# Optimization experiments

Hardware: AMD Instinct MI355X
Metric: run time of the kernel (lower is better)

## Reference

```python
import jax, jax.numpy as jnp
import numpy as np

DIM = 768
N_HEADS = 12
HEAD_DIM = DIM // N_HEADS
B, T = 2, 2048


def setup_inputs() -> dict:
    key = jax.random.key(0)
    ks = jax.random.split(key, 11)
    s = 0.02
    return {
        "q_in": jax.random.normal(ks[0], (B, T, DIM), jnp.float32),
        "k_in": jax.random.normal(ks[1], (B, T, DIM), jnp.float32),
        "v_in": jax.random.normal(ks[2], (B, T, DIM), jnp.float32),
        "Wq": jax.random.normal(ks[3], (DIM, DIM), jnp.float32) * s,
        "bq": jnp.zeros((DIM,), jnp.float32),
        "Wk": jax.random.normal(ks[4], (DIM, DIM), jnp.float32) * s,
        "bk": jnp.zeros((DIM,), jnp.float32),
        "Wv": jax.random.normal(ks[5], (DIM, DIM), jnp.float32) * s,
        "bv": jnp.zeros((DIM,), jnp.float32),
        "Wo": jax.random.normal(ks[6], (DIM, DIM), jnp.float32) * s,
        "bo": jnp.zeros((DIM,), jnp.float32),
    }


def reference(q_in, k_in, v_in, Wq, bq, Wk, bk, Wv, bv, Wo, bo):
    b, t, c = q_in.shape
    scale = HEAD_DIM ** -0.5
    # linear projections (torch Linear: x @ W.T + b)
    q = q_in @ Wq.T + bq
    k = k_in @ Wk.T + bk
    v = v_in @ Wv.T + bv
    # [b, t, h, d] -> [b, h, t, d]
    q = q.reshape(b, t, N_HEADS, HEAD_DIM).transpose(0, 2, 1, 3)
    k = k.reshape(b, t, N_HEADS, HEAD_DIM).transpose(0, 2, 1, 3)
    v = v.reshape(b, t, N_HEADS, HEAD_DIM).transpose(0, 2, 1, 3)
    scores = jnp.einsum("bhqd,bhkd->bhqk", q, k) * scale  # full TxT scores
    probs = jax.nn.softmax(scores, axis=-1)
    attn = jnp.einsum("bhqk,bhkd->bhqd", probs, v)
    attn = attn.transpose(0, 2, 1, 3).reshape(b, t, c)
    return attn @ Wo.T + bo
```

## Files before the change

### kernel.cpp

```cpp
#include <hip/hip_runtime.h>


typedef unsigned short u16;
typedef __attribute__((ext_vector_type(8))) short short8;
typedef __attribute__((ext_vector_type(4))) float float4v;

#define DIMC 768
#define NTOK 4096
#define NHD  12
#define HDD  64
#define SEQT 2048

__device__ __forceinline__ u16 f2bf(float f) {
  union { float f; unsigned u; } v; v.f = f;
  unsigned r = v.u + 0x7fffu + ((v.u >> 16) & 1u);
  return (u16)(r >> 16);
}
__device__ __forceinline__ float bf2f(u16 u) {
  union { unsigned u; float f; } v; v.u = ((unsigned)u) << 16;
  return v.f;
}

__global__ __launch_bounds__(256) void cvt3_kernel(
    const float* __restrict__ a, const float* __restrict__ b, const float* __restrict__ c,
    u16* __restrict__ oa, u16* __restrict__ ob, u16* __restrict__ oc) {
  int z = blockIdx.y;
  const float* s = (z == 0) ? a : (z == 1) ? b : c;
  u16* d = (z == 0) ? oa : (z == 1) ? ob : oc;
  size_t i = ((size_t)blockIdx.x * 256 + threadIdx.x) * 4;
  float4 v = *(const float4*)(s + i);
  *(ushort4*)(d + i) = make_ushort4(f2bf(v.x), f2bf(v.y), f2bf(v.z), f2bf(v.w));
}

__global__ __launch_bounds__(256) void cvt4_kernel(
    const float* __restrict__ a, const float* __restrict__ b,
    const float* __restrict__ c, const float* __restrict__ e,
    u16* __restrict__ oa, u16* __restrict__ ob, u16* __restrict__ oc, u16* __restrict__ oe) {
  int z = blockIdx.y;
  const float* s = (z == 0) ? a : (z == 1) ? b : (z == 2) ? c : e;
  u16* d = (z == 0) ? oa : (z == 1) ? ob : (z == 2) ? oc : oe;
  size_t i = ((size_t)blockIdx.x * 256 + threadIdx.x) * 4;
  float4 v = *(const float4*)(s + i);
  *(ushort4*)(d + i) = make_ushort4(f2bf(v.x), f2bf(v.y), f2bf(v.z), f2bf(v.w));
}

__device__ __forceinline__ void gemm_mainloop2(
    const u16* __restrict__ X, const u16* __restrict__ W,
    int m0, int n0, u16* Als, u16* Bls, float4v acc[4][2]) {
  int tid = threadIdx.x;
  int sr = tid >> 3, sc = (tid & 7) * 8;
  int w = tid >> 6, lane = tid & 63, quad = lane >> 4, r15 = lane & 15;
  int wm = (w >> 1) * 64, wn = (w & 1) * 32;
  const u16* xp0 = X + (size_t)(m0 + sr) * DIMC + sc;
  const u16* xp1 = xp0 + 32 * DIMC;
  const u16* xp2 = xp0 + 64 * DIMC;
  const u16* xp3 = xp0 + 96 * DIMC;
  const u16* wp0 = W + (size_t)(n0 + sr) * DIMC + sc;
  const u16* wp1 = wp0 + 32 * DIMC;
  uint4 pa0 = *(const uint4*)xp0, pa1 = *(const uint4*)xp1;
  uint4 pa2 = *(const uint4*)xp2, pa3 = *(const uint4*)xp3;
  uint4 pb0 = *(const uint4*)wp0, pb1 = *(const uint4*)wp1;
  for (int k0 = 0; k0 < DIMC; k0 += 64) {
    __syncthreads();
    *(uint4*)(Als + sr * 72 + sc) = pa0;
    *(uint4*)(Als + (sr + 32) * 72 + sc) = pa1;
    *(uint4*)(Als + (sr + 64) * 72 + sc) = pa2;
    *(uint4*)(Als + (sr + 96) * 72 + sc) = pa3;
    *(uint4*)(Bls + sr * 72 + sc) = pb0;
    *(uint4*)(Bls + (sr + 32) * 72 + sc) = pb1;
    __syncthreads();
    int kn = k0 + 64;
    if (kn < DIMC) {
      pa0 = *(const uint4*)(xp0 + kn); pa1 = *(const uint4*)(xp1 + kn);
      pa2 = *(const uint4*)(xp2 + kn); pa3 = *(const uint4*)(xp3 + kn);
      pb0 = *(const uint4*)(wp0 + kn); pb1 = *(const uint4*)(wp1 + kn);
    }
    #pragma unroll
    for (int sk = 0; sk < 2; sk++) {
      short8 af[4], bf[2];
      #pragma unroll
      for (int mf = 0; mf < 4; mf++)
        af[mf] = *(const short8*)(Als + (wm + mf * 16 + r15) * 72 + sk * 32 + quad * 8);
      #pragma unroll
      for (int nf = 0; nf < 2; nf++)
        bf[nf] = *(const short8*)(Bls + (wn + nf * 16 + r15) * 72 + sk * 32 + quad * 8);
      #pragma unroll
      for (int mf = 0; mf < 4; mf++)
        #pragma unroll
        for (int nf = 0; nf < 2; nf++)
          acc[mf][nf] = __builtin_amdgcn_mfma_f32_16x16x32_bf16(af[mf], bf[nf], acc[mf][nf], 0, 0, 0);
    }
  }
}

__global__ __launch_bounds__(256, 4) void gemm_qkv(
    const u16* __restrict__ xq, const u16* __restrict__ xk, const u16* __restrict__ xv,
    const u16* __restrict__ wq, const u16* __restrict__ wk, const u16* __restrict__ wv,
    const float* __restrict__ bq, const float* __restrict__ bk, const float* __restrict__ bv,
    u16* __restrict__ Qh, u16* __restrict__ Kh, u16* __restrict__ Vt) {
  __shared__ __align__(16) u16 Als[128 * 72];
  __shared__ __align__(16) u16 Bls[64 * 72];
  int z = blockIdx.z;
  const u16* X = (z == 0) ? xq : (z == 1) ? xk : xv;
  const u16* W = (z == 0) ? wq : (z == 1) ? wk : wv;
  const float* bias = (z == 0) ? bq : (z == 1) ? bk : bv;
  int m0 = blockIdx.x * 128, n0 = blockIdx.y * 64;
  float4v acc[4][2];
  #pragma unroll
  for (int i = 0; i < 4; i++)
    #pragma unroll
    for (int j = 0; j < 2; j++)
      #pragma unroll
      for (int r = 0; r < 4; r++) acc[i][j][r] = 0.f;
  gemm_mainloop2(X, W, m0, n0, Als, Bls, acc);
  int tid = threadIdx.x, w = tid >> 6, lane = tid & 63, quad = lane >> 4, r15 = lane & 15;
  int wm = (w >> 1) * 64, wn = (w & 1) * 32;
  #pragma unroll
  for (int mf = 0; mf < 4; mf++)
    #pragma unroll
    for (int nf = 0; nf < 2; nf++)
      #pragma unroll
      for (int rg = 0; rg < 4; rg++) {
        int m = m0 + wm + mf * 16 + quad * 4 + rg;
        int n = n0 + wn + nf * 16 + r15;
        float val = acc[mf][nf][rg] + bias[n];
        int b = m >> 11, t = m & 2047, h = n >> 6, d = n & 63;
        u16 o = f2bf(val);
        size_t bh = (size_t)(b * NHD + h);
        if (z == 2) Vt[(bh * HDD + d) * SEQT + t] = o;
        else if (z == 0) Qh[(bh * SEQT + t) * HDD + d] = o;
        else Kh[(bh * SEQT + t) * HDD + d] = o;
      }
}

__global__ __launch_bounds__(256, 3) void attn_kernel(
    const u16* __restrict__ Qh, const u16* __restrict__ Kh, const u16* __restrict__ Vt,
    u16* __restrict__ Opart, float* __restrict__ Lpart) {
  constexpr float CEXP = 0.125f * 1.44269504088896f;
  __shared__ __align__(16) u16 Kls[64 * 72];
  __shared__ __align__(16) u16 Vls[64 * 72];
  __shared__ __align__(16) u16 Pls[4 * 32 * 72];
  int bh = blockIdx.y, kv = blockIdx.z, qt0 = blockIdx.x * 128;
  int tid = threadIdx.x, w = tid >> 6, lane = tid & 63, quad = lane >> 4, r15 = lane & 15;
  int qw = qt0 + w * 32;

  short8 qa[2][2];
  #pragma unroll
  for (int qs = 0; qs < 2; qs++) {
    const u16* qp = Qh + ((size_t)bh * SEQT + qw + qs * 16 + r15) * HDD + quad * 8;
    qa[qs][0] = *(const short8*)qp;
    qa[qs][1] = *(const short8*)(qp + 32);
  }
  short8 ones;
  #pragma unroll
  for (int i = 0; i < 8; i++) ones[i] = (short)0x3F80;

  float4v oacc[2][4], lacc[2];
  #pragma unroll
  for (int qs = 0; qs < 2; qs++) {
    #pragma unroll
    for (int r = 0; r < 4; r++) lacc[qs][r] = 0.f;
    #pragma unroll
    for (int dt = 0; dt < 4; dt++)
      #pragma unroll
      for (int r = 0; r < 4; r++) oacc[qs][dt][r] = 0.f;
  }

  const u16* Kbase = Kh + (size_t)bh * SEQT * HDD;
  const u16* Vbase = Vt + (size_t)bh * HDD * SEQT;
  u16* Pw = Pls + w * (32 * 72);
  int sr = tid >> 3, sc = (tid & 7) * 8;
  int kt0 = kv * 1024;

  uint4 pk0 = *(const uint4*)(Kbase + (size_t)(kt0 + sr) * HDD + sc);
  uint4 pk1 = *(const uint4*)(Kbase + (size_t)(kt0 + sr + 32) * HDD + sc);
  uint4 pv0 = *(const uint4*)(Vbase + (size_t)sr * SEQT + kt0 + sc);
  uint4 pv1 = *(const uint4*)(Vbase + (size_t)(sr + 32) * SEQT + kt0 + sc);

  for (int it = 0; it < 16; it++) {
    __syncthreads();
    *(uint4*)(Kls + sr * 72 + sc) = pk0;
    *(uint4*)(Kls + (sr + 32) * 72 + sc) = pk1;
    *(uint4*)(Vls + sr * 72 + sc) = pv0;
    *(uint4*)(Vls + (sr + 32) * 72 + sc) = pv1;
    __syncthreads();
    int ktn = kt0 + ((it + 1) & 15) * 64;
    pk0 = *(const uint4*)(Kbase + (size_t)(ktn + sr) * HDD + sc);
    pk1 = *(const uint4*)(Kbase + (size_t)(ktn + sr + 32) * HDD + sc);
    pv0 = *(const uint4*)(Vbase + (size_t)sr * SEQT + ktn + sc);
    pv1 = *(const uint4*)(Vbase + (size_t)(sr + 32) * SEQT + ktn + sc);

    float4v st[4][2];
    #pragma unroll
    for (int nk = 0; nk < 4; nk++) {
      short8 k0 = *(const short8*)(Kls + (nk * 16 + r15) * 72 + quad * 8);
      short8 k1 = *(const short8*)(Kls + (nk * 16 + r15) * 72 + 32 + quad * 8);
      #pragma unroll
      for (int qs = 0; qs < 2; qs++) {
        float4v z;
        #pragma unroll
        for (int r = 0; r < 4; r++) z[r] = 0.f;
        z = __builtin_amdgcn_mfma_f32_16x16x32_bf16(k0, qa[qs][0], z, 0, 0, 0);
        z = __builtin_amdgcn_mfma_f32_16x16x32_bf16(k1, qa[qs][1], z, 0, 0, 0);
        st[nk][qs] = z;
      }
    }
    #pragma unroll
    for (int qs = 0; qs < 2; qs++)
      #pragma unroll
      for (int nk = 0; nk < 4; nk++) {
        float p0 = exp2f(st[nk][qs][0] * CEXP);
        float p1 = exp2f(st[nk][qs][1] * CEXP);
        float p2 = exp2f(st[nk][qs][2] * CEXP);
        float p3 = exp2f(st[nk][qs][3] * CEXP);
        unsigned lo = __builtin_amdgcn_perm(__float_as_uint(p1), __float_as_uint(p0), 0x07060302u);
        unsigned hi = __builtin_amdgcn_perm(__float_as_uint(p3), __float_as_uint(p2), 0x07060302u);
        *(uint2*)(Pw + (qs * 16 + r15) * 72 + nk * 16 + quad * 4) = make_uint2(lo, hi);
      }
    short8 pa[2][2];
    #pragma unroll
    for (int qs = 0; qs < 2; qs++) {
      pa[qs][0] = *(const short8*)(Pw + (qs * 16 + r15) * 72 + quad * 8);
      pa[qs][1] = *(const short8*)(Pw + (qs * 16 + r15) * 72 + 32 + quad * 8);
      lacc[qs] = __builtin_amdgcn_mfma_f32_16x16x32_bf16(pa[qs][0], ones, lacc[qs], 0, 0, 0);
      lacc[qs] = __builtin_amdgcn_mfma_f32_16x16x32_bf16(pa[qs][1], ones, lacc[qs], 0, 0, 0);
    }
    #pragma unroll
    for (int dt = 0; dt < 4; dt++) {
      short8 v0 = *(const short8*)(Vls + (dt * 16 + r15) * 72 + quad * 8);
      short8 v1 = *(const short8*)(Vls + (dt * 16 + r15) * 72 + 32 + quad * 8);
      #pragma unroll
      for (int qs = 0; qs < 2; qs++) {
        oacc[qs][dt] = __builtin_amdgcn_mfma_f32_16x16x32_bf16(pa[qs][0], v0, oacc[qs][dt], 0, 0, 0);
        oacc[qs][dt] = __builtin_amdgcn_mfma_f32_16x16x32_bf16(pa[qs][1], v1, oacc[qs][dt], 0, 0, 0);
      }
    }
  }
  size_t obase = ((size_t)kv * 2 * NHD + bh) * SEQT;
  #pragma unroll
  for (int qs = 0; qs < 2; qs++)
    #pragma unroll
    for (int rg = 0; rg < 4; rg++) {
      int q = qw + qs * 16 + quad * 4 + rg;
      u16* orow = Opart + (obase + q) * HDD;
      #pragma unroll
      for (int dt = 0; dt < 4; dt++) orow[dt * 16 + r15] = f2bf(oacc[qs][dt][rg]);
      if (r15 == 0) Lpart[obase + q] = lacc[qs][rg];
    }
}

__global__ __launch_bounds__(256) void merge_kernel(
    const u16* __restrict__ Opart, const float* __restrict__ Lpart, u16* __restrict__ X2) {
  int tid = threadIdx.x;
  int row = blockIdx.x * 32 + (tid >> 3);
  int dcol = (tid & 7) * 8;
  int bh = row >> 11, t = row & 2047;
  size_t off1 = (size_t)row * HDD + dcol;
  size_t off2 = off1 + (size_t)2 * NHD * SEQT * HDD;
  ushort4 a0 = *(const ushort4*)(Opart + off1);
  ushort4 a1 = *(const ushort4*)(Opart + off1 + 4);
  ushort4 b0 = *(const ushort4*)(Opart + off2);
  ushort4 b1 = *(const ushort4*)(Opart + off2 + 4);
  float inv = 1.0f / (Lpart[row] + Lpart[row + 2 * NHD * SEQT]);
  int b = bh / NHD, h = bh % NHD;
  u16 o[8];
  o[0] = f2bf((bf2f(a0.x) + bf2f(b0.x)) * inv);
  o[1] = f2bf((bf2f(a0.y) + bf2f(b0.y)) * inv);
  o[2] = f2bf((bf2f(a0.z) + bf2f(b0.z)) * inv);
  o[3] = f2bf((bf2f(a0.w) + bf2f(b0.w)) * inv);
  o[4] = f2bf((bf2f(a1.x) + bf2f(b1.x)) * inv);
  o[5] = f2bf((bf2f(a1.y) + bf2f(b1.y)) * inv);
  o[6] = f2bf((bf2f(a1.z) + bf2f(b1.z)) * inv);
  o[7] = f2bf((bf2f(a1.w) + bf2f(b1.w)) * inv);
  *(uint4*)(X2 + ((size_t)b * SEQT + t) * DIMC + h * HDD + dcol) = *(uint4*)o;
}

__global__ __launch_bounds__(256, 4) void gemm_out(
    const u16* __restrict__ X2, const u16* __restrict__ wo,
    const float* __restrict__ bo, float* __restrict__ out) {
  __shared__ __align__(16) u16 Als[128 * 72];
  __shared__ __align__(16) u16 Bls[64 * 72];
  int m0 = blockIdx.x * 128, n0 = blockIdx.y * 64;
  float4v acc[4][2];
  #pragma unroll
  for (int i = 0; i < 4; i++)
    #pragma unroll
    for (int j = 0; j < 2; j++)
      #pragma unroll
      for (int r = 0; r < 4; r++) acc[i][j][r] = 0.f;
  gemm_mainloop2(X2, wo, m0, n0, Als, Bls, acc);
  int tid = threadIdx.x, w = tid >> 6, lane = tid & 63, quad = lane >> 4, r15 = lane & 15;
  int wm = (w >> 1) * 64, wn = (w & 1) * 32;
  #pragma unroll
  for (int mf = 0; mf < 4; mf++)
    #pragma unroll
    for (int nf = 0; nf < 2; nf++)
      #pragma unroll
      for (int rg = 0; rg < 4; rg++) {
        int m = m0 + wm + mf * 16 + quad * 4 + rg;
        int n = n0 + wn + nf * 16 + r15;
        out[(size_t)m * DIMC + n] = acc[mf][nf][rg] + bo[n];
      }
}

extern "C" void kernel_launch(void* const* d_in, const int* in_sizes, int n_in,
                              void* d_out, int out_size, void* d_ws, size_t ws_size,
                              hipStream_t stream) {
  const float* q_in = (const float*)d_in[0];
  const float* k_in = (const float*)d_in[1];
  const float* v_in = (const float*)d_in[2];
  const float* Wq = (const float*)d_in[3];
  const float* bq = (const float*)d_in[4];
  const float* Wk = (const float*)d_in[5];
  const float* bk = (const float*)d_in[6];
  const float* Wv = (const float*)d_in[7];
  const float* bv = (const float*)d_in[8];
  const float* Wo = (const float*)d_in[9];
  const float* bo = (const float*)d_in[10];

  const size_t NX = (size_t)NTOK * DIMC;
  const size_t NW = (size_t)DIMC * DIMC;
  u16* ws = (u16*)d_ws;
  u16* qb = ws;
  u16* kb = qb + NX;
  u16* vb = kb + NX;
  u16* wqb = vb + NX;
  u16* wkb = wqb + NW;
  u16* wvb = wkb + NW;
  u16* wob = wvb + NW;
  u16* Qh = wob + NW;
  u16* Kh = Qh + NX;
  u16* Vt = Kh + NX;
  u16* X2 = Vt + NX;
  u16* Opart = qb;
  float* Lpart = (float*)(ws + 2 * NX);

  cvt3_kernel<<<dim3(NX / 1024, 3), 256, 0, stream>>>(q_in, k_in, v_in, qb, kb, vb);
  cvt4_kernel<<<dim3(NW / 1024, 4), 256, 0, stream>>>(Wq, Wk, Wv, Wo, wqb, wkb, wvb, wob);
  gemm_qkv<<<dim3(NTOK / 128, DIMC / 64, 3), 256, 0, stream>>>(
      qb, kb, vb, wqb, wkb, wvb, bq, bk, bv, Qh, Kh, Vt);
  attn_kernel<<<dim3(SEQT / 128, 2 * NHD, 2), 256, 0, stream>>>(Qh, Kh, Vt, Opart, Lpart);
  merge_kernel<<<dim3(2 * NHD * SEQT / 32), 256, 0, stream>>>(Opart, Lpart, X2);
  gemm_out<<<dim3(NTOK / 128, DIMC / 64), 256, 0, stream>>>(X2, wob, bo, (float*)d_out);
}
```

Before: 199.9 us.

## Split attention KV into three chunks, fold softmax scale into Q, merge convert kernels

Splits the key range of the attention kernel into three chunks (704/704/640 keys) instead of two, raising the grid from 768 to 1152 blocks for better CU fill, and extends the merge kernel to sum three partials. The softmax scale and log2e factor are folded into the Q projection epilogue, removing a multiply per score. The two conversion kernels are fused into one launch with bounds checks, and the Q-tile launch-bounds occupancy hint is dropped. Costs include more partial-output traffic in the merge and a different rounding point for the scaled Q in bf16.

```diff
diff --git a/kernel.cpp b/kernel.cpp
--- a/kernel.cpp
+++ b/kernel.cpp
@@ -10,6 +10,7 @@
 #define NHD  12
 #define HDD  64
 #define SEQT 2048
+#define CEXPQ 0.1803368757f
 
 __device__ __forceinline__ u16 f2bf(float f) {
   union { float f; unsigned u; } v; v.f = f;
@@ -21,25 +22,25 @@
   return v.f;
 }
 
-__global__ __launch_bounds__(256) void cvt3_kernel(
-    const float* __restrict__ a, const float* __restrict__ b, const float* __restrict__ c,
-    u16* __restrict__ oa, u16* __restrict__ ob, u16* __restrict__ oc) {
+__global__ __launch_bounds__(256) void cvt_all(
+    const float* __restrict__ i0, const float* __restrict__ i1, const float* __restrict__ i2,
+    const float* __restrict__ w0, const float* __restrict__ w1,
+    const float* __restrict__ w2, const float* __restrict__ w3,
+    u16* __restrict__ o0, u16* __restrict__ o1, u16* __restrict__ o2,
+    u16* __restrict__ p0, u16* __restrict__ p1, u16* __restrict__ p2, u16* __restrict__ p3) {
   int z = blockIdx.y;
-  const float* s = (z == 0) ? a : (z == 1) ? b : c;
-  u16* d = (z == 0) ? oa : (z == 1) ? ob : oc;
+  const float* s; u16* d; size_t lim;
+  switch (z) {
+    case 0: s = i0; d = o0; lim = (size_t)NTOK * DIMC; break;
+    case 1: s = i1; d = o1; lim = (size_t)NTOK * DIMC; break;
+    case 2: s = i2; d = o2; lim = (size_t)NTOK * DIMC; break;
+    case 3: s = w0; d = p0; lim = (size_t)DIMC * DIMC; break;
+    case 4: s = w1; d = p1; lim = (size_t)DIMC * DIMC; break;
+    case 5: s = w2; d = p2; lim = (size_t)DIMC * DIMC; break;
+    default: s = w3; d = p3; lim = (size_t)DIMC * DIMC; break;
+  }
   size_t i = ((size_t)blockIdx.x * 256 + threadIdx.x) * 4;
-  float4 v = *(const float4*)(s + i);
-  *(ushort4*)(d + i) = make_ushort4(f2bf(v.x), f2bf(v.y), f2bf(v.z), f2bf(v.w));
-}
-
-__global__ __launch_bounds__(256) void cvt4_kernel(
-    const float* __restrict__ a, const float* __restrict__ b,
-    const float* __restrict__ c, const float* __restrict__ e,
-    u16* __restrict__ oa, u16* __restrict__ ob, u16* __restrict__ oc, u16* __restrict__ oe) {
-  int z = blockIdx.y;
-  const float* s = (z == 0) ? a : (z == 1) ? b : (z == 2) ? c : e;
-  u16* d = (z == 0) ? oa : (z == 1) ? ob : (z == 2) ? oc : oe;
-  size_t i = ((size_t)blockIdx.x * 256 + threadIdx.x) * 4;
+  if (i >= lim) return;
   float4 v = *(const float4*)(s + i);
   *(ushort4*)(d + i) = make_ushort4(f2bf(v.x), f2bf(v.y), f2bf(v.z), f2bf(v.w));
 }
@@ -124,6 +125,7 @@
         int m = m0 + wm + mf * 16 + quad * 4 + rg;
         int n = n0 + wn + nf * 16 + r15;
         float val = acc[mf][nf][rg] + bias[n];
+        if (z == 0) val *= CEXPQ;
         int b = m >> 11, t = m & 2047, h = n >> 6, d = n & 63;
         u16 o = f2bf(val);
         size_t bh = (size_t)(b * NHD + h);
@@ -133,16 +135,17 @@
       }
 }
 
-__global__ __launch_bounds__(256, 3) void attn_kernel(
+__global__ __launch_bounds__(256) void attn_kernel(
     const u16* __restrict__ Qh, const u16* __restrict__ Kh, const u16* __restrict__ Vt,
     u16* __restrict__ Opart, float* __restrict__ Lpart) {
-  constexpr float CEXP = 0.125f * 1.44269504088896f;
   __shared__ __align__(16) u16 Kls[64 * 72];
   __shared__ __align__(16) u16 Vls[64 * 72];
   __shared__ __align__(16) u16 Pls[4 * 32 * 72];
   int bh = blockIdx.y, kv = blockIdx.z, qt0 = blockIdx.x * 128;
   int tid = threadIdx.x, w = tid >> 6, lane = tid & 63, quad = lane >> 4, r15 = lane & 15;
   int qw = qt0 + w * 32;
+  int kt0 = kv * 704;
+  int nit = (kv == 2) ? 10 : 11;
 
   short8 qa[2][2];
   #pragma unroll
@@ -166,29 +169,28 @@
       for (int r = 0; r < 4; r++) oacc[qs][dt][r] = 0.f;
   }
 
-  const u16* Kbase = Kh + (size_t)bh * SEQT * HDD;
-  const u16* Vbase = Vt + (size_t)bh * HDD * SEQT;
   u16* Pw = Pls + w * (32 * 72);
   int sr = tid >> 3, sc = (tid & 7) * 8;
-  int kt0 = kv * 1024;
-
-  uint4 pk0 = *(const uint4*)(Kbase + (size_t)(kt0 + sr) * HDD + sc);
-  uint4 pk1 = *(const uint4*)(Kbase + (size_t)(kt0 + sr + 32) * HDD + sc);
-  uint4 pv0 = *(const uint4*)(Vbase + (size_t)sr * SEQT + kt0 + sc);
-  uint4 pv1 = *(const uint4*)(Vbase + (size_t)(sr + 32) * SEQT + kt0 + sc);
-
-  for (int it = 0; it < 16; it++) {
+  const u16* pK0 = Kh + (size_t)bh * SEQT * HDD + (size_t)(kt0 + sr) * HDD + sc;
+  const u16* pK1 = pK0 + 32 * HDD;
+  const u16* pV0 = Vt + (size_t)bh * HDD * SEQT + (size_t)sr * SEQT + kt0 + sc;
+  const u16* pV1 = pV0 + 32 * SEQT;
+
+  uint4 pk0 = *(const uint4*)pK0, pk1 = *(const uint4*)pK1;
+  uint4 pv0 = *(const uint4*)pV0, pv1 = *(const uint4*)pV1;
+
+  for (int it = 0; it < nit; it++) {
     __syncthreads();
     *(uint4*)(Kls + sr * 72 + sc) = pk0;
     *(uint4*)(Kls + (sr + 32) * 72 + sc) = pk1;
     *(uint4*)(Vls + sr * 72 + sc) = pv0;
     *(uint4*)(Vls + (sr + 32) * 72 + sc) = pv1;
     __syncthreads();
-    int ktn = kt0 + ((it + 1) & 15) * 64;
-    pk0 = *(const uint4*)(Kbase + (size_t)(ktn + sr) * HDD + sc);
-    pk1 = *(const uint4*)(Kbase + (size_t)(ktn + sr + 32) * HDD + sc);
-    pv0 = *(const uint4*)(Vbase + (size_t)sr * SEQT + ktn + sc);
-    pv1 = *(const uint4*)(Vbase + (size_t)(sr + 32) * SEQT + ktn + sc);
+    if (it + 1 < nit) {
+      pK0 += 64 * HDD; pK1 += 64 * HDD; pV0 += 64; pV1 += 64;
+      pk0 = *(const uint4*)pK0; pk1 = *(const uint4*)pK1;
+      pv0 = *(const uint4*)pV0; pv1 = *(const uint4*)pV1;
+    }
 
     float4v st[4][2];
     #pragma unroll
@@ -209,10 +211,10 @@
     for (int qs = 0; qs < 2; qs++)
       #pragma unroll
       for (int nk = 0; nk < 4; nk++) {
-        float p0 = exp2f(st[nk][qs][0] * CEXP);
-        float p1 = exp2f(st[nk][qs][1] * CEXP);
-        float p2 = exp2f(st[nk][qs][2] * CEXP);
-        float p3 = exp2f(st[nk][qs][3] * CEXP);
+        float p0 = exp2f(st[nk][qs][0]);
+        float p1 = exp2f(st[nk][qs][1]);
+        float p2 = exp2f(st[nk][qs][2]);
+        float p3 = exp2f(st[nk][qs][3]);
         unsigned lo = __builtin_amdgcn_perm(__float_as_uint(p1), __float_as_uint(p0), 0x07060302u);
         unsigned hi = __builtin_amdgcn_perm(__float_as_uint(p3), __float_as_uint(p2), 0x07060302u);
         *(uint2*)(Pw + (qs * 16 + r15) * 72 + nk * 16 + quad * 4) = make_uint2(lo, hi);
@@ -251,27 +253,27 @@
 
 __global__ __launch_bounds__(256) void merge_kernel(
     const u16* __restrict__ Opart, const float* __restrict__ Lpart, u16* __restrict__ X2) {
+  const int KVSTR = 2 * NHD * SEQT;
   int tid = threadIdx.x;
   int row = blockIdx.x * 32 + (tid >> 3);
   int dcol = (tid & 7) * 8;
   int bh = row >> 11, t = row & 2047;
-  size_t off1 = (size_t)row * HDD + dcol;
-  size_t off2 = off1 + (size_t)2 * NHD * SEQT * HDD;
-  ushort4 a0 = *(const ushort4*)(Opart + off1);
-  ushort4 a1 = *(const ushort4*)(Opart + off1 + 4);
-  ushort4 b0 = *(const ushort4*)(Opart + off2);
-  ushort4 b1 = *(const ushort4*)(Opart + off2 + 4);
-  float inv = 1.0f / (Lpart[row] + Lpart[row + 2 * NHD * SEQT]);
+  float inv = 1.0f / (Lpart[row] + Lpart[row + KVSTR] + Lpart[row + 2 * KVSTR]);
+  float s[8];
+  #pragma unroll
+  for (int i = 0; i < 8; i++) s[i] = 0.f;
+  #pragma unroll
+  for (int kv = 0; kv < 3; kv++) {
+    size_t off = ((size_t)kv * KVSTR + row) * HDD + dcol;
+    ushort4 a0 = *(const ushort4*)(Opart + off);
+    ushort4 a1 = *(const ushort4*)(Opart + off + 4);
+    s[0] += bf2f(a0.x); s[1] += bf2f(a0.y); s[2] += bf2f(a0.z); s[3] += bf2f(a0.w);
+    s[4] += bf2f(a1.x); s[5] += bf2f(a1.y); s[6] += bf2f(a1.z); s[7] += bf2f(a1.w);
+  }
   int b = bh / NHD, h = bh % NHD;
   u16 o[8];
-  o[0] = f2bf((bf2f(a0.x) + bf2f(b0.x)) * inv);
-  o[1] = f2bf((bf2f(a0.y) + bf2f(b0.y)) * inv);
-  o[2] = f2bf((bf2f(a0.z) + bf2f(b0.z)) * inv);
-  o[3] = f2bf((bf2f(a0.w) + bf2f(b0.w)) * inv);
-  o[4] = f2bf((bf2f(a1.x) + bf2f(b1.x)) * inv);
-  o[5] = f2bf((bf2f(a1.y) + bf2f(b1.y)) * inv);
-  o[6] = f2bf((bf2f(a1.z) + bf2f(b1.z)) * inv);
-  o[7] = f2bf((bf2f(a1.w) + bf2f(b1.w)) * inv);
+  #pragma unroll
+  for (int i = 0; i < 8; i++) o[i] = f2bf(s[i] * inv);
   *(uint4*)(X2 + ((size_t)b * SEQT + t) * DIMC + h * HDD + dcol) = *(uint4*)o;
 }
 
@@ -333,13 +335,13 @@
   u16* Vt = Kh + NX;
   u16* X2 = Vt + NX;
   u16* Opart = qb;
-  float* Lpart = (float*)(ws + 2 * NX);
-
-  cvt3_kernel<<<dim3(NX / 1024, 3), 256, 0, stream>>>(q_in, k_in, v_in, qb, kb, vb);
-  cvt4_kernel<<<dim3(NW / 1024, 4), 256, 0, stream>>>(Wq, Wk, Wv, Wo, wqb, wkb, wvb, wob);
+  float* Lpart = (float*)(X2 + NX);
+
+  cvt_all<<<dim3(NX / 1024, 7), 256, 0, stream>>>(
+      q_in, k_in, v_in, Wq, Wk, Wv, Wo, qb, kb, vb, wqb, wkb, wvb, wob);
   gemm_qkv<<<dim3(NTOK / 128, DIMC / 64, 3), 256, 0, stream>>>(
       qb, kb, vb, wqb, wkb, wvb, bq, bk, bv, Qh, Kh, Vt);
-  attn_kernel<<<dim3(SEQT / 128, 2 * NHD, 2), 256, 0, stream>>>(Qh, Kh, Vt, Opart, Lpart);
+  attn_kernel<<<dim3(SEQT / 128, 2 * NHD, 3), 256, 0, stream>>>(Qh, Kh, Vt, Opart, Lpart);
   merge_kernel<<<dim3(2 * NHD * SEQT / 32), 256, 0, stream>>>(Opart, Lpart, X2);
   gemm_out<<<dim3(NTOK / 128, DIMC / 64), 256, 0, stream>>>(X2, wob, bo, (float*)d_out);
 }
```

After: 215.3 us. 7.7% more time.

## Fuse fp32-to-bf16 conversion into QKV GEMM loads and prescale Q

Applied to the files above, without the earlier changes.

Removes the separate conversion kernels for the activations and the Q/K/V weights. The QKV GEMM now loads fp32 directly, converts to bf16 in registers and stores it to shared memory, which saves a full bf16 write and re-read pass. The softmax scale times log2(e) is folded into the Q projection epilogue, so attention no longer multiplies each score. Attention's launch-bounds occupancy hint is dropped and the workspace layout is rearranged. The cost is twice the global load bytes and more prefetch registers in the QKV GEMM, with Q rounded to bf16 after scaling.

```diff
diff --git a/kernel.cpp b/kernel.cpp
--- a/kernel.cpp
+++ b/kernel.cpp
@@ -1,4 +1,5 @@
 #include <hip/hip_runtime.h>
+#include <hip/hip_bf16.h>
 
 
 typedef unsigned short u16;
@@ -10,6 +11,7 @@
 #define NHD  12
 #define HDD  64
 #define SEQT 2048
+#define CEXPQ 0.1803368757f
 
 __device__ __forceinline__ u16 f2bf(float f) {
   union { float f; unsigned u; } v; v.f = f;
@@ -20,91 +22,40 @@
   union { unsigned u; float f; } v; v.u = ((unsigned)u) << 16;
   return v.f;
 }
-
-__global__ __launch_bounds__(256) void cvt3_kernel(
-    const float* __restrict__ a, const float* __restrict__ b, const float* __restrict__ c,
-    u16* __restrict__ oa, u16* __restrict__ ob, u16* __restrict__ oc) {
-  int z = blockIdx.y;
-  const float* s = (z == 0) ? a : (z == 1) ? b : c;
-  u16* d = (z == 0) ? oa : (z == 1) ? ob : oc;
+__device__ __forceinline__ unsigned pkbf(float a, float b) {
+  __hip_bfloat162 h = __float22bfloat162_rn(make_float2(a, b));
+  return *(unsigned*)&h;
+}
+__device__ __forceinline__ uint4 cv8(float4 lo, float4 hi) {
+  uint4 r;
+  r.x = pkbf(lo.x, lo.y); r.y = pkbf(lo.z, lo.w);
+  r.z = pkbf(hi.x, hi.y); r.w = pkbf(hi.z, hi.w);
+  return r;
+}
+
+__global__ __launch_bounds__(256) void cvt_wo(const float* __restrict__ s, u16* __restrict__ d) {
   size_t i = ((size_t)blockIdx.x * 256 + threadIdx.x) * 4;
   float4 v = *(const float4*)(s + i);
   *(ushort4*)(d + i) = make_ushort4(f2bf(v.x), f2bf(v.y), f2bf(v.z), f2bf(v.w));
 }
 
-__global__ __launch_bounds__(256) void cvt4_kernel(
-    const float* __restrict__ a, const float* __restrict__ b,
-    const float* __restrict__ c, const float* __restrict__ e,
-    u16* __restrict__ oa, u16* __restrict__ ob, u16* __restrict__ oc, u16* __restrict__ oe) {
-  int z = blockIdx.y;
-  const float* s = (z == 0) ? a : (z == 1) ? b : (z == 2) ? c : e;
-  u16* d = (z == 0) ? oa : (z == 1) ? ob : (z == 2) ? oc : oe;
-  size_t i = ((size_t)blockIdx.x * 256 + threadIdx.x) * 4;
-  float4 v = *(const float4*)(s + i);
-  *(ushort4*)(d + i) = make_ushort4(f2bf(v.x), f2bf(v.y), f2bf(v.z), f2bf(v.w));
-}
-
-__device__ __forceinline__ void gemm_mainloop2(
-    const u16* __restrict__ X, const u16* __restrict__ W,
-    int m0, int n0, u16* Als, u16* Bls, float4v acc[4][2]) {
-  int tid = threadIdx.x;
-  int sr = tid >> 3, sc = (tid & 7) * 8;
-  int w = tid >> 6, lane = tid & 63, quad = lane >> 4, r15 = lane & 15;
-  int wm = (w >> 1) * 64, wn = (w & 1) * 32;
-  const u16* xp0 = X + (size_t)(m0 + sr) * DIMC + sc;
-  const u16* xp1 = xp0 + 32 * DIMC;
-  const u16* xp2 = xp0 + 64 * DIMC;
-  const u16* xp3 = xp0 + 96 * DIMC;
-  const u16* wp0 = W + (size_t)(n0 + sr) * DIMC + sc;
-  const u16* wp1 = wp0 + 32 * DIMC;
-  uint4 pa0 = *(const uint4*)xp0, pa1 = *(const uint4*)xp1;
-  uint4 pa2 = *(const uint4*)xp2, pa3 = *(const uint4*)xp3;
-  uint4 pb0 = *(const uint4*)wp0, pb1 = *(const uint4*)wp1;
-  for (int k0 = 0; k0 < DIMC; k0 += 64) {
-    __syncthreads();
-    *(uint4*)(Als + sr * 72 + sc) = pa0;
-    *(uint4*)(Als + (sr + 32) * 72 + sc) = pa1;
-    *(uint4*)(Als + (sr + 64) * 72 + sc) = pa2;
-    *(uint4*)(Als + (sr + 96) * 72 + sc) = pa3;
-    *(uint4*)(Bls + sr * 72 + sc) = pb0;
-    *(uint4*)(Bls + (sr + 32) * 72 + sc) = pb1;
-    __syncthreads();
-    int kn = k0 + 64;
-    if (kn < DIMC) {
-      pa0 = *(const uint4*)(xp0 + kn); pa1 = *(const uint4*)(xp1 + kn);
-      pa2 = *(const uint4*)(xp2 + kn); pa3 = *(const uint4*)(xp3 + kn);
-      pb0 = *(const uint4*)(wp0 + kn); pb1 = *(const uint4*)(wp1 + kn);
-    }
-    #pragma unroll
-    for (int sk = 0; sk < 2; sk++) {
-      short8 af[4], bf[2];
-      #pragma unroll
-      for (int mf = 0; mf < 4; mf++)
-        af[mf] = *(const short8*)(Als + (wm + mf * 16 + r15) * 72 + sk * 32 + quad * 8);
-      #pragma unroll
-      for (int nf = 0; nf < 2; nf++)
-        bf[nf] = *(const short8*)(Bls + (wn + nf * 16 + r15) * 72 + sk * 32 + quad * 8);
-      #pragma unroll
-      for (int mf = 0; mf < 4; mf++)
-        #pragma unroll
-        for (int nf = 0; nf < 2; nf++)
-          acc[mf][nf] = __builtin_amdgcn_mfma_f32_16x16x32_bf16(af[mf], bf[nf], acc[mf][nf], 0, 0, 0);
-    }
-  }
-}
-
 __global__ __launch_bounds__(256, 4) void gemm_qkv(
-    const u16* __restrict__ xq, const u16* __restrict__ xk, const u16* __restrict__ xv,
-    const u16* __restrict__ wq, const u16* __restrict__ wk, const u16* __restrict__ wv,
+    const float* __restrict__ xq, const float* __restrict__ xk, const float* __restrict__ xv,
+    const float* __restrict__ wq, const float* __restrict__ wk, const float* __restrict__ wv,
     const float* __restrict__ bq, const float* __restrict__ bk, const float* __restrict__ bv,
     u16* __restrict__ Qh, u16* __restrict__ Kh, u16* __restrict__ Vt) {
   __shared__ __align__(16) u16 Als[128 * 72];
   __shared__ __align__(16) u16 Bls[64 * 72];
   int z = blockIdx.z;
-  const u16* X = (z == 0) ? xq : (z == 1) ? xk : xv;
-  const u16* W = (z == 0) ? wq : (z == 1) ? wk : wv;
+  const float* X = (z == 0) ? xq : (z == 1) ? xk : xv;
+  const float* W = (z == 0) ? wq : (z == 1) ? wk : wv;
   const float* bias = (z == 0) ? bq : (z == 1) ? bk : bv;
   int m0 = blockIdx.x * 128, n0 = blockIdx.y * 64;
+  int tid = threadIdx.x;
+  int sr = tid >> 3, sc = (tid & 7) * 8;
+  int w = tid >> 6, lane = tid & 63, quad = lane >> 4, r15 = lane & 15;
+  int wm = (w >> 1) * 64, wn = (w & 1) * 32;
+
   float4v acc[4][2];
   #pragma unroll
   for (int i = 0; i < 4; i++)
@@ -112,9 +63,62 @@
     for (int j = 0; j < 2; j++)
       #pragma unroll
       for (int r = 0; r < 4; r++) acc[i][j][r] = 0.f;
-  gemm_mainloop2(X, W, m0, n0, Als, Bls, acc);
-  int tid = threadIdx.x, w = tid >> 6, lane = tid & 63, quad = lane >> 4, r15 = lane & 15;
-  int wm = (w >> 1) * 64, wn = (w & 1) * 32;
+
+  const float* xp0 = X + (size_t)(m0 + sr) * DIMC + sc;
+  const float* xp1 = xp0 + 32 * DIMC;
+  const float* xp2 = xp0 + 64 * DIMC;
+  const float* xp3 = xp0 + 96 * DIMC;
+  const float* wp0 = W + (size_t)(n0 + sr) * DIMC + sc;
+  const float* wp1 = wp0 + 32 * DIMC;
+  float4 pa[4][2], pb[2][2];
+  #pragma unroll
+  for (int r = 0; r < 4; r++) {
+    const float* p = (r == 0) ? xp0 : (r == 1) ? xp1 : (r == 2) ? xp2 : xp3;
+    pa[r][0] = *(const float4*)p; pa[r][1] = *(const float4*)(p + 4);
+  }
+  pb[0][0] = *(const float4*)wp0; pb[0][1] = *(const float4*)(wp0 + 4);
+  pb[1][0] = *(const float4*)wp1; pb[1][1] = *(const float4*)(wp1 + 4);
+
+  for (int k0 = 0; k0 < DIMC; k0 += 64) {
+    uint4 ca0 = cv8(pa[0][0], pa[0][1]);
+    uint4 ca1 = cv8(pa[1][0], pa[1][1]);
+    uint4 ca2 = cv8(pa[2][0], pa[2][1]);
+    uint4 ca3 = cv8(pa[3][0], pa[3][1]);
+    uint4 cb0 = cv8(pb[0][0], pb[0][1]);
+    uint4 cb1 = cv8(pb[1][0], pb[1][1]);
+    __syncthreads();
+    *(uint4*)(Als + sr * 72 + sc) = ca0;
+    *(uint4*)(Als + (sr + 32) * 72 + sc) = ca1;
+    *(uint4*)(Als + (sr + 64) * 72 + sc) = ca2;
+    *(uint4*)(Als + (sr + 96) * 72 + sc) = ca3;
+    *(uint4*)(Bls + sr * 72 + sc) = cb0;
+    *(uint4*)(Bls + (sr + 32) * 72 + sc) = cb1;
+    __syncthreads();
+    int kn = k0 + 64;
+    if (kn < DIMC) {
+      pa[0][0] = *(const float4*)(xp0 + kn); pa[0][1] = *(const float4*)(xp0 + kn + 4);
+      pa[1][0] = *(const float4*)(xp1 + kn); pa[1][1] = *(const float4*)(xp1 + kn + 4);
+      pa[2][0] = *(const float4*)(xp2 + kn); pa[2][1] = *(const float4*)(xp2 + kn + 4);
+      pa[3][0] = *(const float4*)(xp3 + kn); pa[3][1] = *(const float4*)(xp3 + kn + 4);
+      pb[0][0] = *(const float4*)(wp0 + kn); pb[0][1] = *(const float4*)(wp0 + kn + 4);
+      pb[1][0] = *(const float4*)(wp1 + kn); pb[1][1] = *(const float4*)(wp1 + kn + 4);
+    }
+    #pragma unroll
+    for (int sk = 0; sk < 2; sk++) {
+      short8 af[4], bf[2];
+      #pragma unroll
+      for (int mf = 0; mf < 4; mf++)
+        af[mf] = *(const short8*)(Als + (wm + mf * 16 + r15) * 72 + sk * 32 + quad * 8);
+      #pragma unroll
+      for (int nf = 0; nf < 2; nf++)
+        bf[nf] = *(const short8*)(Bls + (wn + nf * 16 + r15) * 72 + sk * 32 + quad * 8);
+      #pragma unroll
+      for (int mf = 0; mf < 4; mf++)
+        #pragma unroll
+        for (int nf = 0; nf < 2; nf++)
+          acc[mf][nf] = __builtin_amdgcn_mfma_f32_16x16x32_bf16(af[mf], bf[nf], acc[mf][nf], 0, 0, 0);
+    }
+  }
   #pragma unroll
   for (int mf = 0; mf < 4; mf++)
     #pragma unroll
@@ -124,6 +128,7 @@
         int m = m0 + wm + mf * 16 + quad * 4 + rg;
         int n = n0 + wn + nf * 16 + r15;
         float val = acc[mf][nf][rg] + bias[n];
+        if (z == 0) val *= CEXPQ;
         int b = m >> 11, t = m & 2047, h = n >> 6, d = n & 63;
         u16 o = f2bf(val);
         size_t bh = (size_t)(b * NHD + h);
@@ -133,10 +138,9 @@
       }
 }
 
-__global__ __launch_bounds__(256, 3) void attn_kernel(
+__global__ __launch_bounds__(256) void attn_kernel(
     const u16* __restrict__ Qh, const u16* __restrict__ Kh, const u16* __restrict__ Vt,
     u16* __restrict__ Opart, float* __restrict__ Lpart) {
-  constexpr float CEXP = 0.125f * 1.44269504088896f;
   __shared__ __align__(16) u16 Kls[64 * 72];
   __shared__ __align__(16) u16 Vls[64 * 72];
   __shared__ __align__(16) u16 Pls[4 * 32 * 72];
@@ -166,16 +170,14 @@
       for (int r = 0; r < 4; r++) oacc[qs][dt][r] = 0.f;
   }
 
-  const u16* Kbase = Kh + (size_t)bh * SEQT * HDD;
-  const u16* Vbase = Vt + (size_t)bh * HDD * SEQT;
   u16* Pw = Pls + w * (32 * 72);
   int sr = tid >> 3, sc = (tid & 7) * 8;
   int kt0 = kv * 1024;
 
-  uint4 pk0 = *(const uint4*)(Kbase + (size_t)(kt0 + sr) * HDD + sc);
-  uint4 pk1 = *(const uint4*)(Kbase + (size_t)(kt0 + sr + 32) * HDD + sc);
-  uint4 pv0 = *(const uint4*)(Vbase + (size_t)sr * SEQT + kt0 + sc);
-  uint4 pv1 = *(const uint4*)(Vbase + (size_t)(sr + 32) * SEQT + kt0 + sc);
+  uint4 pk0 = *(const uint4*)(Kh + (size_t)bh * SEQT * HDD + (size_t)(kt0 + sr) * HDD + sc);
+  uint4 pk1 = *(const uint4*)(Kh + (size_t)bh * SEQT * HDD + (size_t)(kt0 + sr + 32) * HDD + sc);
+  uint4 pv0 = *(const uint4*)(Vt + (size_t)bh * HDD * SEQT + (size_t)sr * SEQT + kt0 + sc);
+  uint4 pv1 = *(const uint4*)(Vt + (size_t)bh * HDD * SEQT + (size_t)(sr + 32) * SEQT + kt0 + sc);
 
   for (int it = 0; it < 16; it++) {
     __syncthreads();
@@ -185,10 +187,10 @@
     *(uint4*)(Vls + (sr + 32) * 72 + sc) = pv1;
     __syncthreads();
     int ktn = kt0 + ((it + 1) & 15) * 64;
-    pk0 = *(const uint4*)(Kbase + (size_t)(ktn + sr) * HDD + sc);
-    pk1 = *(const uint4*)(Kbase + (size_t)(ktn + sr + 32) * HDD + sc);
-    pv0 = *(const uint4*)(Vbase + (size_t)sr * SEQT + ktn + sc);
-    pv1 = *(const uint4*)(Vbase + (size_t)(sr + 32) * SEQT + ktn + sc);
+    pk0 = *(const uint4*)(Kh + (size_t)bh * SEQT * HDD + (size_t)(ktn + sr) * HDD + sc);
+    pk1 = *(const uint4*)(Kh + (size_t)bh * SEQT * HDD + (size_t)(ktn + sr + 32) * HDD + sc);
+    pv0 = *(const uint4*)(Vt + (size_t)bh * HDD * SEQT + (size_t)sr * SEQT + ktn + sc);
+    pv1 = *(const uint4*)(Vt + (size_t)bh * HDD * SEQT + (size_t)(sr + 32) * SEQT + ktn + sc);
 
     float4v st[4][2];
     #pragma unroll
@@ -209,10 +211,10 @@
     for (int qs = 0; qs < 2; qs++)
       #pragma unroll
       for (int nk = 0; nk < 4; nk++) {
-        float p0 = exp2f(st[nk][qs][0] * CEXP);
-        float p1 = exp2f(st[nk][qs][1] * CEXP);
-        float p2 = exp2f(st[nk][qs][2] * CEXP);
-        float p3 = exp2f(st[nk][qs][3] * CEXP);
+        float p0 = exp2f(st[nk][qs][0]);
+        float p1 = exp2f(st[nk][qs][1]);
+        float p2 = exp2f(st[nk][qs][2]);
+        float p3 = exp2f(st[nk][qs][3]);
         unsigned lo = __builtin_amdgcn_perm(__float_as_uint(p1), __float_as_uint(p0), 0x07060302u);
         unsigned hi = __builtin_amdgcn_perm(__float_as_uint(p3), __float_as_uint(p2), 0x07060302u);
         *(uint2*)(Pw + (qs * 16 + r15) * 72 + nk * 16 + quad * 4) = make_uint2(lo, hi);
@@ -281,6 +283,11 @@
   __shared__ __align__(16) u16 Als[128 * 72];
   __shared__ __align__(16) u16 Bls[64 * 72];
   int m0 = blockIdx.x * 128, n0 = blockIdx.y * 64;
+  int tid = threadIdx.x;
+  int sr = tid >> 3, sc = (tid & 7) * 8;
+  int w = tid >> 6, lane = tid & 63, quad = lane >> 4, r15 = lane & 15;
+  int wm = (w >> 1) * 64, wn = (w & 1) * 32;
+
   float4v acc[4][2];
   #pragma unroll
   for (int i = 0; i < 4; i++)
@@ -288,9 +295,47 @@
     for (int j = 0; j < 2; j++)
       #pragma unroll
       for (int r = 0; r < 4; r++) acc[i][j][r] = 0.f;
-  gemm_mainloop2(X2, wo, m0, n0, Als, Bls, acc);
-  int tid = threadIdx.x, w = tid >> 6, lane = tid & 63, quad = lane >> 4, r15 = lane & 15;
-  int wm = (w >> 1) * 64, wn = (w & 1) * 32;
+
+  const u16* xp0 = X2 + (size_t)(m0 + sr) * DIMC + sc;
+  const u16* xp1 = xp0 + 32 * DIMC;
+  const u16* xp2 = xp0 + 64 * DIMC;
+  const u16* xp3 = xp0 + 96 * DIMC;
+  const u16* wp0 = wo + (size_t)(n0 + sr) * DIMC + sc;
+  const u16* wp1 = wp0 + 32 * DIMC;
+  uint4 pa0 = *(const uint4*)xp0, pa1 = *(const uint4*)xp1;
+  uint4 pa2 = *(const uint4*)xp2, pa3 = *(const uint4*)xp3;
+  uint4 pb0 = *(const uint4*)wp0, pb1 = *(const uint4*)wp1;
+  for (int k0 = 0; k0 < DIMC; k0 += 64) {
+    __syncthreads();
+    *(uint4*)(Als + sr * 72 + sc) = pa0;
+    *(uint4*)(Als + (sr + 32) * 72 + sc) = pa1;
+    *(uint4*)(Als + (sr + 64) * 72 + sc) = pa2;
+    *(uint4*)(Als + (sr + 96) * 72 + sc) = pa3;
+    *(uint4*)(Bls + sr * 72 + sc) = pb0;
+    *(uint4*)(Bls + (sr + 32) * 72 + sc) = pb1;
+    __syncthreads();
+    int kn = k0 + 64;
+    if (kn < DIMC) {
+      pa0 = *(const uint4*)(xp0 + kn); pa1 = *(const uint4*)(xp1 + kn);
+      pa2 = *(const uint4*)(xp2 + kn); pa3 = *(const uint4*)(xp3 + kn);
+      pb0 = *(const uint4*)(wp0 + kn); pb1 = *(const uint4*)(wp1 + kn);
+    }
+    #pragma unroll
+    for (int sk = 0; sk < 2; sk++) {
+      short8 af[4], bf[2];
+      #pragma unroll
+      for (int mf = 0; mf < 4; mf++)
+        af[mf] = *(const short8*)(Als + (wm + mf * 16 + r15) * 72 + sk * 32 + quad * 8);
+      #pragma unroll
+      for (int nf = 0; nf < 2; nf++)
+        bf[nf] = *(const short8*)(Bls + (wn + nf * 16 + r15) * 72 + sk * 32 + quad * 8);
+      #pragma unroll
+      for (int mf = 0; mf < 4; mf++)
+        #pragma unroll
+        for (int nf = 0; nf < 2; nf++)
+          acc[mf][nf] = __builtin_amdgcn_mfma_f32_16x16x32_bf16(af[mf], bf[nf], acc[mf][nf], 0, 0, 0);
+    }
+  }
   #pragma unroll
   for (int mf = 0; mf < 4; mf++)
     #pragma unroll
@@ -321,24 +366,17 @@
   const size_t NX = (size_t)NTOK * DIMC;
   const size_t NW = (size_t)DIMC * DIMC;
   u16* ws = (u16*)d_ws;
-  u16* qb = ws;
-  u16* kb = qb + NX;
-  u16* vb = kb + NX;
-  u16* wqb = vb + NX;
-  u16* wkb = wqb + NW;
-  u16* wvb = wkb + NW;
-  u16* wob = wvb + NW;
-  u16* Qh = wob + NW;
+  u16* Qh = ws;
   u16* Kh = Qh + NX;
   u16* Vt = Kh + NX;
   u16* X2 = Vt + NX;
-  u16* Opart = qb;
-  float* Lpart = (float*)(ws + 2 * NX);
-
-  cvt3_kernel<<<dim3(NX / 1024, 3), 256, 0, stream>>>(q_in, k_in, v_in, qb, kb, vb);
-  cvt4_kernel<<<dim3(NW / 1024, 4), 256, 0, stream>>>(Wq, Wk, Wv, Wo, wqb, wkb, wvb, wob);
+  u16* wob = X2 + NX;
+  u16* Opart = wob + NW;
+  float* Lpart = (float*)(Opart + 2 * NX);
+
+  cvt_wo<<<dim3(NW / 1024), 256, 0, stream>>>(Wo, wob);
   gemm_qkv<<<dim3(NTOK / 128, DIMC / 64, 3), 256, 0, stream>>>(
-      qb, kb, vb, wqb, wkb, wvb, bq, bk, bv, Qh, Kh, Vt);
+      q_in, k_in, v_in, Wq, Wk, Wv, bq, bk, bv, Qh, Kh, Vt);
   attn_kernel<<<dim3(SEQT / 128, 2 * NHD, 2), 256, 0, stream>>>(Qh, Kh, Vt, Opart, Lpart);
   merge_kernel<<<dim3(2 * NHD * SEQT / 32), 256, 0, stream>>>(Opart, Lpart, X2);
   gemm_out<<<dim3(NTOK / 128, DIMC / 64), 256, 0, stream>>>(X2, wob, bo, (float*)d_out);
```

Result: slower. 216.4 us (+8.2%).
